# Kernel optimization log

Hardware: AMD Instinct MI355X
Metric: run time of the kernel (lower is better)

The kernel has to match this reference:

```python
import jax, jax.numpy as jnp
import numpy as np

T, B, C, H = 2048, 2, 1024, 16
DK = C // H


def setup_inputs() -> dict:
    key = jax.random.key(0)
    ks = jax.random.split(key, 12)
    s = 1.0 / np.sqrt(C)
    return {
        "query": jax.random.normal(ks[0], (T, B, C), jnp.float32),
        "key": jax.random.normal(ks[1], (T, B, C), jnp.float32),
        "value": jax.random.normal(ks[2], (T, B, C), jnp.float32),
        "Wq": jax.random.normal(ks[3], (C, C), jnp.float32) * s,
        "bq": jnp.zeros((C,), jnp.float32),
        "Wk": jax.random.normal(ks[4], (C, C), jnp.float32) * s,
        "bk": jnp.zeros((C,), jnp.float32),
        "Wv": jax.random.normal(ks[5], (C, C), jnp.float32) * s,
        "bv": jnp.zeros((C,), jnp.float32),
        "Wo": jax.random.normal(ks[6], (C, C), jnp.float32) * s,
        "bo": jnp.zeros((C,), jnp.float32),
        "key_padding_mask": jax.random.randint(ks[7], (B, T), 0, 2).astype(jnp.bool_),
    }


def reference(query, key, value, Wq, bq, Wk, bk, Wv, bv, Wo, bo, key_padding_mask):
    # T,B,C -> B,T,C
    q_in = jnp.transpose(query, (1, 0, 2))
    k_in = jnp.transpose(key, (1, 0, 2))
    v_in = jnp.transpose(value, (1, 0, 2))
    nb = q_in.shape[0]
    # linear projections, split heads: B,T,C -> B,H,T,dk
    def proj(x, W, b):
        y = x @ W.T + b
        return jnp.transpose(y.reshape(nb, -1, H, DK), (0, 2, 1, 3))
    q = proj(q_in, Wq, bq)
    k = proj(k_in, Wk, bk)
    v = proj(v_in, Wv, bv)
    # scores: B,H,T1,T2
    scores = jnp.einsum("bhqd,bhkd->bhqk", q, k) / np.sqrt(DK).astype(np.float32)
    scores = jnp.where(key_padding_mask[:, None, None, :], -jnp.inf, scores)
    attn = jax.nn.softmax(scores, axis=-1)
    # context: B,H,T1,dk -> B,T1,C
    x = jnp.einsum("bhqk,bhkd->bhqd", attn, v)
    x = jnp.transpose(x, (0, 2, 1, 3)).reshape(nb, -1, H * DK)
    out = x @ Wo.T + bo
    # B,T,C -> T,B,C
    return jnp.transpose(out, (1, 0, 2))
```

## Files before the change

kernel.cpp:

```cpp
#include <hip/hip_runtime.h>
#include <stdint.h>

typedef __attribute__((ext_vector_type(4))) float f32x4;
typedef __attribute__((ext_vector_type(16))) float f32x16;
typedef __attribute__((ext_vector_type(8))) short bf16x8;
typedef __attribute__((ext_vector_type(2))) unsigned int u32x2;
typedef __attribute__((ext_vector_type(4))) unsigned int u32x4;
typedef unsigned short u16;
typedef unsigned int u32;

#define DEVINL __device__ __forceinline__

DEVINL u16 f2bf(float f) {
  u32 u = __builtin_bit_cast(u32, f);
  u += 0x7FFFu + ((u >> 16) & 1u);
  return (u16)(u >> 16);
}

DEVINL float exp2_hw(float x) {
  float r;
  asm("v_exp_f32 %0, %1\n\ts_nop 0" : "=v"(r) : "v"(x));
  return r;
}

DEVINL u32 cvt_pk_bf16(float lo, float hi) {
  u32 r;
  asm("v_cvt_pk_bf16_f32 %0, %1, %2" : "=v"(r) : "v"(lo), "v"(hi));
  return r;
}

DEVINL void gload16(const void* g, void* l) {
  __builtin_amdgcn_global_load_lds((const __attribute__((address_space(1))) void*)g,
                                   (__attribute__((address_space(3))) void*)l, 16, 0, 0);
}

DEVINL void wait_vm0() { asm volatile("s_waitcnt vmcnt(0)" ::: "memory"); }
DEVINL void wait_vm3() { asm volatile("s_waitcnt vmcnt(3)" ::: "memory"); }
DEVINL void wait_vm4() { asm volatile("s_waitcnt vmcnt(4)" ::: "memory"); }
#define SBAR0 __builtin_amdgcn_sched_barrier(0)

__global__ void cvt_all(const float* __restrict__ q, const float* __restrict__ k,
                        const float* __restrict__ v, const float* __restrict__ wq,
                        const float* __restrict__ wk, const float* __restrict__ wv,
                        const float* __restrict__ wo, ushort4* __restrict__ dst,
                        const u32* __restrict__ mraw, float* __restrict__ mout) {
  if (blockIdx.x == 16384) {
    __shared__ int notint, notfloat;
    int tid = threadIdx.x;
    if (tid == 0) { notint = 0; notfloat = 0; }
    __syncthreads();
    for (int i = tid; i < 1024; i += 256) {
      u32 w = mraw[i];
      if (w != 0u && w != 1u) notint = 1;
      if (w != 0u && w != 0x3f800000u) notfloat = 1;
    }
    __syncthreads();
    bool words = (!notint) || (!notfloat);
    for (int i = tid; i < 4096; i += 256) {
      u32 vv = words ? mraw[i] : (u32)(((const unsigned char*)mraw)[i]);
      mout[i] = vv ? -1.0e38f : -8.0f;
    }
    return;
  }
  int i = blockIdx.x * 256 + threadIdx.x;
  float4 v4;
  if (i < 1048576) v4 = ((const float4*)q)[i];
  else if (i < 2097152) v4 = ((const float4*)k)[i - 1048576];
  else if (i < 3145728) v4 = ((const float4*)v)[i - 2097152];
  else {
    int j = i - 3145728;
    if (j < 262144) v4 = ((const float4*)wq)[j];
    else if (j < 524288) v4 = ((const float4*)wk)[j - 262144];
    else if (j < 786432) v4 = ((const float4*)wv)[j - 524288];
    else v4 = ((const float4*)wo)[j - 786432];
  }
  ushort4 o;
  o.x = f2bf(v4.x); o.y = f2bf(v4.y); o.z = f2bf(v4.z); o.w = f2bf(v4.w);
  dst[i] = o;
}

DEVINL void gemm_body(const u16* __restrict__ A, const u16* __restrict__ W,
                      const float* __restrict__ bias, u16* __restrict__ out_bf,
                      int tile, int mode, float scale, u16* As, u16* Bs) {
  const int tid = threadIdx.x, lane = tid & 63;
  const int wave = tid >> 6, wm = wave & 1, wn = wave >> 1;
  const int m0 = (tile >> 3) << 7;
  const int n0 = (tile & 7) << 7;
  const int l15 = lane & 15, l4 = lane >> 4;
  const int K = 1024;
  const f32x4 zero = {0.f, 0.f, 0.f, 0.f};
  f32x4 acc[4][4];
#pragma unroll
  for (int i = 0; i < 4; i++)
#pragma unroll
    for (int j = 0; j < 4; j++) acc[i][j] = zero;

  auto stage = [&](int buf, int kti) {
    u16* Ab = As + buf * 4096;
    u16* Bb = Bs + buf * 4096;
#pragma unroll
    for (int it = 0; it < 2; ++it) {
      int c = tid + (it << 8);
      int row = c >> 2, qs = (c & 3) ^ ((row & 3) ^ ((row >> 2) & 3));
      gload16(A + (size_t)(m0 + row) * K + kti * 32 + qs * 8, (void*)(Ab + c * 8));
      gload16(W + (size_t)(n0 + row) * K + kti * 32 + qs * 8, (void*)(Bb + c * 8));
    }
  };

  stage(0, 0);
  stage(1, 1);

  for (int kti = 0; kti < 32; ++kti) {
    const int cur = kti % 3;
    if (kti == 31) wait_vm0(); else wait_vm4();
    __builtin_amdgcn_s_barrier();
    SBAR0;
    if (kti < 30) stage((kti + 2) % 3, kti + 2);

    const u16* Ac = As + cur * 4096;
    const u16* Bc = Bs + cur * 4096;
    bf16x8 af[4], bfr[4];
#pragma unroll
    for (int i = 0; i < 4; i++) {
      int ra = (wm << 6) + (i << 4) + l15;
      int rb = (wn << 6) + (i << 4) + l15;
      af[i]  = *(const bf16x8*)(Ac + ra * 32 + ((l4 * 8) ^ ((((ra & 3) ^ ((ra >> 2) & 3))) << 3)));
      bfr[i] = *(const bf16x8*)(Bc + rb * 32 + ((l4 * 8) ^ ((((rb & 3) ^ ((rb >> 2) & 3))) << 3)));
    }
    __builtin_amdgcn_s_setprio(1);
#pragma unroll
    for (int i = 0; i < 4; i++)
#pragma unroll
      for (int j = 0; j < 4; j++)
        acc[i][j] = __builtin_amdgcn_mfma_f32_16x16x32_bf16(af[i], bfr[j], acc[i][j], 0, 0, 0);
    __builtin_amdgcn_s_setprio(0);
  }

#pragma unroll
  for (int j = 0; j < 4; j++) {
    const int col = n0 + (wn << 6) + (j << 4) + l15;
    const float bc = bias[col];
#pragma unroll
    for (int i = 0; i < 4; i++) {
#pragma unroll
      for (int r = 0; r < 4; r++) {
        const int row = m0 + (wm << 6) + (i << 4) + (l4 << 2) + r;
        float v = (acc[i][j][r] + bc) * scale;
        int t = row >> 1, b2 = row & 1, h = col >> 6, dh = col & 63;
        if (mode == 2)
          out_bf[((size_t)(b2 * 16 + h) * 64 + dh) * 2048 + t] = f2bf(v);
        else
          out_bf[((size_t)(b2 * 16 + h) * 2048 + t) * 64 + dh] = f2bf(v);
      }
    }
  }
}

__global__ __launch_bounds__(256, 3) void gemm_qkv(
    const u16* __restrict__ qbf, const u16* __restrict__ kbf, const u16* __restrict__ vbf,
    const u16* __restrict__ wq, const u16* __restrict__ wk, const u16* __restrict__ wv,
    const float* __restrict__ bq, const float* __restrict__ bk, const float* __restrict__ bv,
    u16* __restrict__ Qh, u16* __restrict__ Kh, u16* __restrict__ Vth) {
  __shared__ __align__(16) u16 As[3 * 4096];
  __shared__ __align__(16) u16 Bs[3 * 4096];
  const float C2 = 0.18033688011112042f;
  int wg = blockIdx.x;
  int swz = (wg & 7) * 96 + (wg >> 3);
  int prob = swz >> 8, tile = swz & 255;
  if (prob == 0)      gemm_body(qbf, wq, bq, Qh,  tile, 0, C2, As, Bs);
  else if (prob == 1) gemm_body(kbf, wk, bk, Kh,  tile, 0, 1.0f, As, Bs);
  else                gemm_body(vbf, wv, bv, Vth, tile, 2, 1.0f, As, Bs);
}

__global__ __launch_bounds__(256, 2) void gemm_o(
    const u16* __restrict__ ctx, const u16* __restrict__ wo,
    const float* __restrict__ bo, float* __restrict__ out) {
  __shared__ __align__(16) u16 As[3 * 2048];
  __shared__ __align__(16) u16 Bs[3 * 4096];
  const int tid = threadIdx.x, lane = tid & 63;
  const int wave = tid >> 6, wm = wave & 1, wn = wave >> 1;
  const int wg = blockIdx.x;
  const int swz = (wg & 7) * 64 + (wg >> 3);
  const int m0 = (swz >> 3) << 6;
  const int n0 = (swz & 7) << 7;
  const int l15 = lane & 15, l4 = lane >> 4;
  const f32x4 zero = {0.f, 0.f, 0.f, 0.f};
  f32x4 acc[2][4];
#pragma unroll
  for (int i = 0; i < 2; i++)
#pragma unroll
    for (int j = 0; j < 4; j++) acc[i][j] = zero;

  auto stage = [&](int buf, int kti) {
    u16* Ab = As + buf * 2048;
    u16* Bb = Bs + buf * 4096;
    {
      int c = tid;
      int row = c >> 2, qs = (c & 3) ^ ((row & 3) ^ ((row >> 2) & 3));
      gload16(ctx + (size_t)(m0 + row) * 1024 + kti * 32 + qs * 8, (void*)(Ab + c * 8));
    }
#pragma unroll
    for (int it = 0; it < 2; ++it) {
      int c = tid + (it << 8);
      int row = c >> 2, qs = (c & 3) ^ ((row & 3) ^ ((row >> 2) & 3));
      gload16(wo + (size_t)(n0 + row) * 1024 + kti * 32 + qs * 8, (void*)(Bb + c * 8));
    }
  };

  stage(0, 0);
  stage(1, 1);

  for (int kti = 0; kti < 32; ++kti) {
    const int cur = kti % 3;
    if (kti == 31) wait_vm0(); else wait_vm3();
    __builtin_amdgcn_s_barrier();
    SBAR0;
    if (kti < 30) stage((kti + 2) % 3, kti + 2);

    const u16* Ac = As + cur * 2048;
    const u16* Bc = Bs + cur * 4096;
    bf16x8 af[2], bfr[4];
#pragma unroll
    for (int i = 0; i < 2; i++) {
      int ra = (wm << 5) + (i << 4) + l15;
      af[i] = *(const bf16x8*)(Ac + ra * 32 + ((l4 * 8) ^ ((((ra & 3) ^ ((ra >> 2) & 3))) << 3)));
    }
#pragma unroll
    for (int j = 0; j < 4; j++) {
      int rb = (wn << 6) + (j << 4) + l15;
      bfr[j] = *(const bf16x8*)(Bc + rb * 32 + ((l4 * 8) ^ ((((rb & 3) ^ ((rb >> 2) & 3))) << 3)));
    }
    __builtin_amdgcn_s_setprio(1);
#pragma unroll
    for (int i = 0; i < 2; i++)
#pragma unroll
      for (int j = 0; j < 4; j++)
        acc[i][j] = __builtin_amdgcn_mfma_f32_16x16x32_bf16(af[i], bfr[j], acc[i][j], 0, 0, 0);
    __builtin_amdgcn_s_setprio(0);
  }

#pragma unroll
  for (int j = 0; j < 4; j++) {
    const int col = n0 + (wn << 6) + (j << 4) + l15;
    const float bc = bo[col];
#pragma unroll
    for (int i = 0; i < 2; i++) {
#pragma unroll
      for (int r = 0; r < 4; r++) {
        const int row = m0 + (wm << 5) + (i << 4) + (l4 << 2) + r;
        float v = acc[i][j][r] + bc;
        int t = row & 2047, b2 = row >> 11;
        out[(size_t)(t * 2 + b2) * 1024 + col] = v;
      }
    }
  }
}

__global__ __launch_bounds__(256, 2) void attn_fwd(
    const u16* __restrict__ Qh, const u16* __restrict__ Kh, const u16* __restrict__ Vt,
    const float* __restrict__ maskf, u16* __restrict__ ctx) {
  __shared__ __align__(16) u16 Ks[3][64 * 64];
  __shared__ __align__(16) u16 Vs[3][64 * 64];
  __shared__ __align__(16) float Ml[2048];
  const int tid = threadIdx.x, lane = tid & 63, wave = tid >> 6;
  const int wg = blockIdx.x;
  const int swz = (wg & 7) * 64 + (wg >> 3);
  const int qt = swz & 15, bh = swz >> 4;
  const int bb = bh >> 4, h = bh & 15;
  const int l31 = lane & 31, hi = lane >> 5;
  const size_t kvbase = (size_t)bh * 2048 * 64;
  const int qbase = qt * 128 + wave * 32;

  gload16(maskf + bb * 2048 + tid * 4, (void*)(&Ml[tid * 4]));
  gload16(maskf + bb * 2048 + 1024 + tid * 4, (void*)(&Ml[1024 + tid * 4]));

  bf16x8 qf[4];
#pragma unroll
  for (int kc = 0; kc < 4; kc++)
    qf[kc] = *(const bf16x8*)(Qh + kvbase + (size_t)(qbase + l31) * 64 + kc * 16 + hi * 8);

  f32x16 zz;
#pragma unroll
  for (int e = 0; e < 16; e++) zz[e] = 0.f;
  f32x16 O[2];
  O[0] = zz; O[1] = zz;
  float l_ = 0.f;

  auto stage = [&](int buf, int kt) {
#pragma unroll
    for (int it = 0; it < 2; ++it) {
      int c = tid + (it << 8);
      int row = c >> 3, qs = (c & 7) ^ (row & 7);
      gload16(Kh + kvbase + (size_t)(kt * 64 + row) * 64 + qs * 8, (void*)(&Ks[buf][c * 8]));
      gload16(Vt + kvbase + (size_t)row * 2048 + kt * 64 + qs * 8, (void*)(&Vs[buf][c * 8]));
    }
  };

  stage(0, 0);
  stage(1, 1);

  for (int kt = 0; kt < 32; ++kt) {
    const int cur = kt % 3;
    if (kt == 31) wait_vm0(); else wait_vm4();
    __builtin_amdgcn_s_barrier();
    SBAR0;
    if (kt < 30) stage((kt + 2) % 3, kt + 2);

    f32x16 s[2];
    s[0] = zz; s[1] = zz;
    __builtin_amdgcn_s_setprio(1);
#pragma unroll
    for (int kc = 0; kc < 4; kc++) {
      const int ch = (((kc * 2 + hi) ^ (l31 & 7)) << 3);
      bf16x8 kf0 = *(const bf16x8*)(&Ks[cur][l31 * 64 + ch]);
      bf16x8 kf1 = *(const bf16x8*)(&Ks[cur][(l31 + 32) * 64 + ch]);
      s[0] = __builtin_amdgcn_mfma_f32_32x32x16_bf16(kf0, qf[kc], s[0], 0, 0, 0);
      s[1] = __builtin_amdgcn_mfma_f32_32x32x16_bf16(kf1, qf[kc], s[1], 0, 0, 0);
    }
    __builtin_amdgcn_s_setprio(0);

    float rs = 0.f;
#pragma unroll
    for (int kb = 0; kb < 2; kb++)
#pragma unroll
      for (int g = 0; g < 4; g++) {
        float4 mv = *(const float4*)(&Ml[kt * 64 + kb * 32 + g * 8 + hi * 4]);
        float p0 = exp2_hw(s[kb][4 * g + 0] + mv.x);
        float p1 = exp2_hw(s[kb][4 * g + 1] + mv.y);
        float p2 = exp2_hw(s[kb][4 * g + 2] + mv.z);
        float p3 = exp2_hw(s[kb][4 * g + 3] + mv.w);
        s[kb][4 * g + 0] = p0; s[kb][4 * g + 1] = p1;
        s[kb][4 * g + 2] = p2; s[kb][4 * g + 3] = p3;
        rs += (p0 + p1) + (p2 + p3);
      }
    rs += __shfl_xor(rs, 32);
    l_ += rs;

    u32 pw[2][8];
#pragma unroll
    for (int kb = 0; kb < 2; kb++)
#pragma unroll
      for (int g = 0; g < 4; g++) {
        pw[kb][2 * g]     = cvt_pk_bf16(s[kb][4 * g + 0], s[kb][4 * g + 1]);
        pw[kb][2 * g + 1] = cvt_pk_bf16(s[kb][4 * g + 2], s[kb][4 * g + 3]);
      }

    __builtin_amdgcn_s_setprio(1);
#pragma unroll
    for (int kc = 0; kc < 4; kc++) {
      const int kb = kc >> 1, m = kc & 1;
      auto r0 = __builtin_amdgcn_permlane32_swap(pw[kb][4 * m + 0], pw[kb][4 * m + 2], false, false);
      auto r1 = __builtin_amdgcn_permlane32_swap(pw[kb][4 * m + 1], pw[kb][4 * m + 3], false, false);
      u32x4 fw = {r0[0], r1[0], r0[1], r1[1]};
      bf16x8 pf = __builtin_bit_cast(bf16x8, fw);
      const int ch = (((kc * 2 + hi) ^ (l31 & 7)) << 3);
      bf16x8 vf0 = *(const bf16x8*)(&Vs[cur][l31 * 64 + ch]);
      bf16x8 vf1 = *(const bf16x8*)(&Vs[cur][(l31 + 32) * 64 + ch]);
      O[0] = __builtin_amdgcn_mfma_f32_32x32x16_bf16(vf0, pf, O[0], 0, 0, 0);
      O[1] = __builtin_amdgcn_mfma_f32_32x32x16_bf16(vf1, pf, O[1], 0, 0, 0);
    }
    __builtin_amdgcn_s_setprio(0);
  }

  float inv = (l_ > 0.f) ? 1.0f / l_ : 0.f;
  const int q = qbase + l31;
  u16* cb = ctx + ((size_t)bb * 2048 + q) * 1024 + h * 64;
#pragma unroll
  for (int nd = 0; nd < 2; nd++)
#pragma unroll
    for (int g = 0; g < 4; g++) {
      u32x2 w;
      w[0] = cvt_pk_bf16(O[nd][4 * g + 0] * inv, O[nd][4 * g + 1] * inv);
      w[1] = cvt_pk_bf16(O[nd][4 * g + 2] * inv, O[nd][4 * g + 3] * inv);
      *(u32x2*)(cb + nd * 32 + g * 8 + hi * 4) = w;
    }
}

extern "C" void kernel_launch(void* const* d_in, const int* in_sizes, int n_in,
                              void* d_out, int out_size, void* d_ws, size_t ws_size,
                              hipStream_t stream) {
  const float* q_in = (const float*)d_in[0];
  const float* k_in = (const float*)d_in[1];
  const float* v_in = (const float*)d_in[2];
  const float* Wq = (const float*)d_in[3];
  const float* bq = (const float*)d_in[4];
  const float* Wk = (const float*)d_in[5];
  const float* bk = (const float*)d_in[6];
  const float* Wv = (const float*)d_in[7];
  const float* bv = (const float*)d_in[8];
  const float* Wo = (const float*)d_in[9];
  const float* bo = (const float*)d_in[10];
  const void* mask = d_in[11];

  const size_t SZ_X = (size_t)4194304 * 2;
  const size_t SZ_W = (size_t)1048576 * 2;
  uint8_t* ws = (uint8_t*)d_ws;
  float* mf = (float*)ws;
  size_t off = 32768;
  u16* qbf = (u16*)(ws + off); off += SZ_X;
  u16* kbf = (u16*)(ws + off); off += SZ_X;
  u16* vbf = (u16*)(ws + off); off += SZ_X;
  u16* wqb = (u16*)(ws + off); off += SZ_W;
  u16* wkb = (u16*)(ws + off); off += SZ_W;
  u16* wvb = (u16*)(ws + off); off += SZ_W;
  u16* wob = (u16*)(ws + off); off += SZ_W;
  u16* Qh  = (u16*)(ws + off); off += SZ_X;
  u16* Kh  = (u16*)(ws + off); off += SZ_X;
  u16* Vth = (u16*)(ws + off); off += SZ_X;
  u16* ctx = (u16*)(ws + off); off += SZ_X;
  if (ws_size < off) return;

  cvt_all<<<16385, 256, 0, stream>>>(q_in, k_in, v_in, Wq, Wk, Wv, Wo,
                                     (ushort4*)qbf, (const u32*)mask, mf);

  gemm_qkv<<<768, 256, 0, stream>>>(qbf, kbf, vbf, wqb, wkb, wvb, bq, bk, bv, Qh, Kh, Vth);

  attn_fwd<<<512, 256, 0, stream>>>(Qh, Kh, Vth, mf, ctx);

  gemm_o<<<512, 256, 0, stream>>>(ctx, wob, bo, (float*)d_out);
}
```

Measured before the change: 134.8 us.

## Rewrite attention kernel with 16x16 MFMA tiles, smaller query blocks, double buffering

The attention kernel moves from 32x32x16 MFMA on 128-query blocks to 16x16x32 MFMA on 64-query blocks, which doubles the grid and raises the launch-bounds occupancy target. The K/V staging ring drops from a triple buffer with vmcnt waits to a double buffer with a full __syncthreads per tile. The probability transpose goes through a per-wave swizzled LDS scratch instead of permlane32 swaps, and the mask is read straight from global memory rather than staged in LDS. The aim is more waves in flight to hide latency. In exchange, each K/V tile is reused across fewer queries, and the kernel adds barriers and LDS round trips.

```diff
diff --git a/kernel.cpp b/kernel.cpp
--- a/kernel.cpp
+++ b/kernel.cpp
@@ -2,7 +2,6 @@
 #include <stdint.h>
 
 typedef __attribute__((ext_vector_type(4))) float f32x4;
-typedef __attribute__((ext_vector_type(16))) float f32x16;
 typedef __attribute__((ext_vector_type(8))) short bf16x8;
 typedef __attribute__((ext_vector_type(2))) unsigned int u32x2;
 typedef __attribute__((ext_vector_type(4))) unsigned int u32x4;
@@ -256,34 +255,29 @@
   }
 }
 
-__global__ __launch_bounds__(256, 2) void attn_fwd(
+__global__ __launch_bounds__(256, 4) void attn_fwd(
     const u16* __restrict__ Qh, const u16* __restrict__ Kh, const u16* __restrict__ Vt,
     const float* __restrict__ maskf, u16* __restrict__ ctx) {
-  __shared__ __align__(16) u16 Ks[3][64 * 64];
-  __shared__ __align__(16) u16 Vs[3][64 * 64];
-  __shared__ __align__(16) float Ml[2048];
+  __shared__ __align__(16) u16 Ks[2][64 * 64];
+  __shared__ __align__(16) u16 Vs[2][64 * 64];
+  __shared__ __align__(16) u32 Plu[4][16 * 32];
   const int tid = threadIdx.x, lane = tid & 63, wave = tid >> 6;
   const int wg = blockIdx.x;
-  const int swz = (wg & 7) * 64 + (wg >> 3);
-  const int qt = swz & 15, bh = swz >> 4;
+  const int swz = (wg & 7) * 128 + (wg >> 3);
+  const int qt = swz & 31, bh = swz >> 5;
   const int bb = bh >> 4, h = bh & 15;
-  const int l31 = lane & 31, hi = lane >> 5;
+  const int l15 = lane & 15, l4 = lane >> 4;
+  const f32x4 zero = {0.f, 0.f, 0.f, 0.f};
   const size_t kvbase = (size_t)bh * 2048 * 64;
-  const int qbase = qt * 128 + wave * 32;
-
-  gload16(maskf + bb * 2048 + tid * 4, (void*)(&Ml[tid * 4]));
-  gload16(maskf + bb * 2048 + 1024 + tid * 4, (void*)(&Ml[1024 + tid * 4]));
-
-  bf16x8 qf[4];
-#pragma unroll
-  for (int kc = 0; kc < 4; kc++)
-    qf[kc] = *(const bf16x8*)(Qh + kvbase + (size_t)(qbase + l31) * 64 + kc * 16 + hi * 8);
-
-  f32x16 zz;
-#pragma unroll
-  for (int e = 0; e < 16; e++) zz[e] = 0.f;
-  f32x16 O[2];
-  O[0] = zz; O[1] = zz;
+
+  bf16x8 qf[2];
+#pragma unroll
+  for (int kb = 0; kb < 2; kb++)
+    qf[kb] = *(const bf16x8*)(Qh + kvbase + (size_t)(qt * 64 + wave * 16 + l15) * 64 + kb * 32 + l4 * 8);
+
+  f32x4 O[4];
+#pragma unroll
+  for (int nd = 0; nd < 4; nd++) O[nd] = zero;
   float l_ = 0.f;
 
   auto stage = [&](int buf, int kt) {
@@ -297,83 +291,83 @@
   };
 
   stage(0, 0);
-  stage(1, 1);
+  __syncthreads();
+
+  const float4* mrow = (const float4*)(maskf + bb * 2048);
 
   for (int kt = 0; kt < 32; ++kt) {
-    const int cur = kt % 3;
-    if (kt == 31) wait_vm0(); else wait_vm4();
-    __builtin_amdgcn_s_barrier();
-    SBAR0;
-    if (kt < 30) stage((kt + 2) % 3, kt + 2);
-
-    f32x16 s[2];
-    s[0] = zz; s[1] = zz;
+    const int cur = kt & 1;
+    if (kt < 31) stage(cur ^ 1, kt + 1);
+
+    f32x4 s[4];
     __builtin_amdgcn_s_setprio(1);
 #pragma unroll
-    for (int kc = 0; kc < 4; kc++) {
-      const int ch = (((kc * 2 + hi) ^ (l31 & 7)) << 3);
-      bf16x8 kf0 = *(const bf16x8*)(&Ks[cur][l31 * 64 + ch]);
-      bf16x8 kf1 = *(const bf16x8*)(&Ks[cur][(l31 + 32) * 64 + ch]);
-      s[0] = __builtin_amdgcn_mfma_f32_32x32x16_bf16(kf0, qf[kc], s[0], 0, 0, 0);
-      s[1] = __builtin_amdgcn_mfma_f32_32x32x16_bf16(kf1, qf[kc], s[1], 0, 0, 0);
+    for (int ni = 0; ni < 4; ni++) {
+      int row = ni * 16 + l15;
+      s[ni] = zero;
+#pragma unroll
+      for (int kb = 0; kb < 2; kb++) {
+        bf16x8 kf = *(const bf16x8*)(&Ks[cur][row * 64 + (((kb * 64 + l4 * 16) ^ ((row & 7) << 4)) >> 1)]);
+        s[ni] = __builtin_amdgcn_mfma_f32_16x16x32_bf16(kf, qf[kb], s[ni], 0, 0, 0);
+      }
     }
     __builtin_amdgcn_s_setprio(0);
 
     float rs = 0.f;
 #pragma unroll
-    for (int kb = 0; kb < 2; kb++)
-#pragma unroll
-      for (int g = 0; g < 4; g++) {
-        float4 mv = *(const float4*)(&Ml[kt * 64 + kb * 32 + g * 8 + hi * 4]);
-        float p0 = exp2_hw(s[kb][4 * g + 0] + mv.x);
-        float p1 = exp2_hw(s[kb][4 * g + 1] + mv.y);
-        float p2 = exp2_hw(s[kb][4 * g + 2] + mv.z);
-        float p3 = exp2_hw(s[kb][4 * g + 3] + mv.w);
-        s[kb][4 * g + 0] = p0; s[kb][4 * g + 1] = p1;
-        s[kb][4 * g + 2] = p2; s[kb][4 * g + 3] = p3;
-        rs += (p0 + p1) + (p2 + p3);
-      }
+    for (int ni = 0; ni < 4; ni++) {
+      float4 mv = mrow[kt * 16 + ni * 4 + l4];
+      float p0 = exp2_hw(s[ni][0] + mv.x);
+      float p1 = exp2_hw(s[ni][1] + mv.y);
+      float p2 = exp2_hw(s[ni][2] + mv.z);
+      float p3 = exp2_hw(s[ni][3] + mv.w);
+      s[ni][0] = p0; s[ni][1] = p1; s[ni][2] = p2; s[ni][3] = p3;
+      rs += (p0 + p1) + (p2 + p3);
+    }
+    rs += __shfl_xor(rs, 16);
     rs += __shfl_xor(rs, 32);
     l_ += rs;
 
-    u32 pw[2][8];
-#pragma unroll
-    for (int kb = 0; kb < 2; kb++)
-#pragma unroll
-      for (int g = 0; g < 4; g++) {
-        pw[kb][2 * g]     = cvt_pk_bf16(s[kb][4 * g + 0], s[kb][4 * g + 1]);
-        pw[kb][2 * g + 1] = cvt_pk_bf16(s[kb][4 * g + 2], s[kb][4 * g + 3]);
+#pragma unroll
+    for (int ni = 0; ni < 4; ni++) {
+      u32x2 w;
+      w.x = cvt_pk_bf16(s[ni][0], s[ni][1]);
+      w.y = cvt_pk_bf16(s[ni][2], s[ni][3]);
+      int col = ni * 8 + l4 * 2;
+      *(u32x2*)(&Plu[wave][l15 * 32 + (col ^ ((l15 & 7) << 2))]) = w;
+    }
+
+    bf16x8 pb[2];
+#pragma unroll
+    for (int kb = 0; kb < 2; kb++) {
+      int rcol = kb * 16 + l4 * 4;
+      pb[kb] = *(const bf16x8*)(&Plu[wave][l15 * 32 + (rcol ^ ((l15 & 7) << 2))]);
+    }
+    __builtin_amdgcn_s_setprio(1);
+#pragma unroll
+    for (int nd = 0; nd < 4; nd++) {
+      int row = nd * 16 + l15;
+#pragma unroll
+      for (int jb = 0; jb < 2; jb++) {
+        bf16x8 vf = *(const bf16x8*)(&Vs[cur][row * 64 + (((jb * 64 + l4 * 16) ^ ((row & 7) << 4)) >> 1)]);
+        O[nd] = __builtin_amdgcn_mfma_f32_16x16x32_bf16(vf, pb[jb], O[nd], 0, 0, 0);
       }
-
-    __builtin_amdgcn_s_setprio(1);
-#pragma unroll
-    for (int kc = 0; kc < 4; kc++) {
-      const int kb = kc >> 1, m = kc & 1;
-      auto r0 = __builtin_amdgcn_permlane32_swap(pw[kb][4 * m + 0], pw[kb][4 * m + 2], false, false);
-      auto r1 = __builtin_amdgcn_permlane32_swap(pw[kb][4 * m + 1], pw[kb][4 * m + 3], false, false);
-      u32x4 fw = {r0[0], r1[0], r0[1], r1[1]};
-      bf16x8 pf = __builtin_bit_cast(bf16x8, fw);
-      const int ch = (((kc * 2 + hi) ^ (l31 & 7)) << 3);
-      bf16x8 vf0 = *(const bf16x8*)(&Vs[cur][l31 * 64 + ch]);
-      bf16x8 vf1 = *(const bf16x8*)(&Vs[cur][(l31 + 32) * 64 + ch]);
-      O[0] = __builtin_amdgcn_mfma_f32_32x32x16_bf16(vf0, pf, O[0], 0, 0, 0);
-      O[1] = __builtin_amdgcn_mfma_f32_32x32x16_bf16(vf1, pf, O[1], 0, 0, 0);
     }
     __builtin_amdgcn_s_setprio(0);
+
+    __syncthreads();
   }
 
   float inv = (l_ > 0.f) ? 1.0f / l_ : 0.f;
-  const int q = qbase + l31;
-  u16* cb = ctx + ((size_t)bb * 2048 + q) * 1024 + h * 64;
-#pragma unroll
-  for (int nd = 0; nd < 2; nd++)
-#pragma unroll
-    for (int g = 0; g < 4; g++) {
-      u32x2 w;
-      w[0] = cvt_pk_bf16(O[nd][4 * g + 0] * inv, O[nd][4 * g + 1] * inv);
-      w[1] = cvt_pk_bf16(O[nd][4 * g + 2] * inv, O[nd][4 * g + 3] * inv);
-      *(u32x2*)(cb + nd * 32 + g * 8 + hi * 4) = w;
-    }
+  int t = qt * 64 + wave * 16 + l15;
+  u16* cb = ctx + ((size_t)bb * 2048 + t) * 1024 + h * 64;
+#pragma unroll
+  for (int nd = 0; nd < 4; nd++) {
+    u32x2 w;
+    w.x = cvt_pk_bf16(O[nd][0] * inv, O[nd][1] * inv);
+    w.y = cvt_pk_bf16(O[nd][2] * inv, O[nd][3] * inv);
+    *(u32x2*)(cb + nd * 16 + l4 * 4) = w;
+  }
 }
 
 extern "C" void kernel_launch(void* const* d_in, const int* in_sizes, int n_in,
@@ -415,7 +409,7 @@
 
   gemm_qkv<<<768, 256, 0, stream>>>(qbf, kbf, vbf, wqb, wkb, wvb, bq, bk, bv, Qh, Kh, Vth);
 
-  attn_fwd<<<512, 256, 0, stream>>>(Qh, Kh, Vth, mf, ctx);
+  attn_fwd<<<1024, 256, 0, stream>>>(Qh, Kh, Vth, mf, ctx);
 
   gemm_o<<<512, 256, 0, stream>>>(ctx, wob, bo, (float*)d_out);
 }
```

Result: slower. 142.8 us (+6.0%).

## Software-pipeline QK^T of next key tile with softmax and PV of current

Applied to the files above, without the earlier changes.

The attention loop is restructured so each iteration issues the QK^T MFMAs for the next key tile before running the exp/softmax and PV MFMAs for the current tile, with two ping-pong score registers. The K/V LDS ring goes from 3 to 4 buffers and prefetch runs three tiles ahead, with wait counts adjusted. The goal is to overlap matrix-core work with the transcendental and conversion ALU work and hide load latency better. In exchange it uses more LDS per block and more accumulator registers, which could cost occupancy or cause spills.

```diff
diff --git a/kernel.cpp b/kernel.cpp
--- a/kernel.cpp
+++ b/kernel.cpp
@@ -37,6 +37,7 @@
 DEVINL void wait_vm0() { asm volatile("s_waitcnt vmcnt(0)" ::: "memory"); }
 DEVINL void wait_vm3() { asm volatile("s_waitcnt vmcnt(3)" ::: "memory"); }
 DEVINL void wait_vm4() { asm volatile("s_waitcnt vmcnt(4)" ::: "memory"); }
+DEVINL void wait_vm8() { asm volatile("s_waitcnt vmcnt(8)" ::: "memory"); }
 #define SBAR0 __builtin_amdgcn_sched_barrier(0)
 
 __global__ void cvt_all(const float* __restrict__ q, const float* __restrict__ k,
@@ -259,8 +260,8 @@
 __global__ __launch_bounds__(256, 2) void attn_fwd(
     const u16* __restrict__ Qh, const u16* __restrict__ Kh, const u16* __restrict__ Vt,
     const float* __restrict__ maskf, u16* __restrict__ ctx) {
-  __shared__ __align__(16) u16 Ks[3][64 * 64];
-  __shared__ __align__(16) u16 Vs[3][64 * 64];
+  __shared__ __align__(16) u16 Ks[4][64 * 64];
+  __shared__ __align__(16) u16 Vs[4][64 * 64];
   __shared__ __align__(16) float Ml[2048];
   const int tid = threadIdx.x, lane = tid & 63, wave = tid >> 6;
   const int wg = blockIdx.x;
@@ -274,18 +275,6 @@
   gload16(maskf + bb * 2048 + tid * 4, (void*)(&Ml[tid * 4]));
   gload16(maskf + bb * 2048 + 1024 + tid * 4, (void*)(&Ml[1024 + tid * 4]));
 
-  bf16x8 qf[4];
-#pragma unroll
-  for (int kc = 0; kc < 4; kc++)
-    qf[kc] = *(const bf16x8*)(Qh + kvbase + (size_t)(qbase + l31) * 64 + kc * 16 + hi * 8);
-
-  f32x16 zz;
-#pragma unroll
-  for (int e = 0; e < 16; e++) zz[e] = 0.f;
-  f32x16 O[2];
-  O[0] = zz; O[1] = zz;
-  float l_ = 0.f;
-
   auto stage = [&](int buf, int kt) {
 #pragma unroll
     for (int it = 0; it < 2; ++it) {
@@ -298,53 +287,71 @@
 
   stage(0, 0);
   stage(1, 1);
-
-  for (int kt = 0; kt < 32; ++kt) {
-    const int cur = kt % 3;
-    if (kt == 31) wait_vm0(); else wait_vm4();
+  stage(2, 2);
+
+  bf16x8 qf[4];
+#pragma unroll
+  for (int kc = 0; kc < 4; kc++)
+    qf[kc] = *(const bf16x8*)(Qh + kvbase + (size_t)(qbase + l31) * 64 + kc * 16 + hi * 8);
+
+  f32x16 zz;
+#pragma unroll
+  for (int e = 0; e < 16; e++) zz[e] = 0.f;
+  f32x16 O[2];
+  O[0] = zz; O[1] = zz;
+  float l_ = 0.f;
+
+  auto qk = [&](int buf, f32x16& s0, f32x16& s1) {
+    s0 = zz; s1 = zz;
+#pragma unroll
+    for (int kc = 0; kc < 4; kc++) {
+      const int ch = (((kc * 2 + hi) ^ (l31 & 7)) << 3);
+      bf16x8 kf0 = *(const bf16x8*)(&Ks[buf][l31 * 64 + ch]);
+      bf16x8 kf1 = *(const bf16x8*)(&Ks[buf][(l31 + 32) * 64 + ch]);
+      s0 = __builtin_amdgcn_mfma_f32_32x32x16_bf16(kf0, qf[kc], s0, 0, 0, 0);
+      s1 = __builtin_amdgcn_mfma_f32_32x32x16_bf16(kf1, qf[kc], s1, 0, 0, 0);
+    }
+  };
+
+  auto iter = [&](int kt, f32x16& c0, f32x16& c1, f32x16& n0, f32x16& n1) {
+    if (kt == 30) wait_vm0(); else wait_vm4();
     __builtin_amdgcn_s_barrier();
     SBAR0;
-    if (kt < 30) stage((kt + 2) % 3, kt + 2);
-
-    f32x16 s[2];
-    s[0] = zz; s[1] = zz;
-    __builtin_amdgcn_s_setprio(1);
-#pragma unroll
-    for (int kc = 0; kc < 4; kc++) {
-      const int ch = (((kc * 2 + hi) ^ (l31 & 7)) << 3);
-      bf16x8 kf0 = *(const bf16x8*)(&Ks[cur][l31 * 64 + ch]);
-      bf16x8 kf1 = *(const bf16x8*)(&Ks[cur][(l31 + 32) * 64 + ch]);
-      s[0] = __builtin_amdgcn_mfma_f32_32x32x16_bf16(kf0, qf[kc], s[0], 0, 0, 0);
-      s[1] = __builtin_amdgcn_mfma_f32_32x32x16_bf16(kf1, qf[kc], s[1], 0, 0, 0);
-    }
-    __builtin_amdgcn_s_setprio(0);
+    if (kt <= 28) stage((kt + 3) & 3, kt + 3);
+    if (kt < 31) qk((kt + 1) & 3, n0, n1);
 
     float rs = 0.f;
-#pragma unroll
-    for (int kb = 0; kb < 2; kb++)
+    f32x16* sp[2] = {&c0, &c1};
+#pragma unroll
+    for (int kb = 0; kb < 2; kb++) {
+      f32x16& s = *sp[kb];
 #pragma unroll
       for (int g = 0; g < 4; g++) {
         float4 mv = *(const float4*)(&Ml[kt * 64 + kb * 32 + g * 8 + hi * 4]);
-        float p0 = exp2_hw(s[kb][4 * g + 0] + mv.x);
-        float p1 = exp2_hw(s[kb][4 * g + 1] + mv.y);
-        float p2 = exp2_hw(s[kb][4 * g + 2] + mv.z);
-        float p3 = exp2_hw(s[kb][4 * g + 3] + mv.w);
-        s[kb][4 * g + 0] = p0; s[kb][4 * g + 1] = p1;
-        s[kb][4 * g + 2] = p2; s[kb][4 * g + 3] = p3;
+        float p0 = exp2_hw(s[4 * g + 0] + mv.x);
+        float p1 = exp2_hw(s[4 * g + 1] + mv.y);
+        float p2 = exp2_hw(s[4 * g + 2] + mv.z);
+        float p3 = exp2_hw(s[4 * g + 3] + mv.w);
+        s[4 * g + 0] = p0; s[4 * g + 1] = p1;
+        s[4 * g + 2] = p2; s[4 * g + 3] = p3;
         rs += (p0 + p1) + (p2 + p3);
       }
+    }
     rs += __shfl_xor(rs, 32);
     l_ += rs;
 
     u32 pw[2][8];
 #pragma unroll
-    for (int kb = 0; kb < 2; kb++)
+    for (int kb = 0; kb < 2; kb++) {
+      f32x16& s = *sp[kb];
 #pragma unroll
       for (int g = 0; g < 4; g++) {
-        pw[kb][2 * g]     = cvt_pk_bf16(s[kb][4 * g + 0], s[kb][4 * g + 1]);
-        pw[kb][2 * g + 1] = cvt_pk_bf16(s[kb][4 * g + 2], s[kb][4 * g + 3]);
+        pw[kb][2 * g]     = cvt_pk_bf16(s[4 * g + 0], s[4 * g + 1]);
+        pw[kb][2 * g + 1] = cvt_pk_bf16(s[4 * g + 2], s[4 * g + 3]);
       }
-
+    }
+
+    const int cur = kt & 3;
     __builtin_amdgcn_s_setprio(1);
 #pragma unroll
     for (int kc = 0; kc < 4; kc++) {
@@ -360,6 +367,17 @@
       O[1] = __builtin_amdgcn_mfma_f32_32x32x16_bf16(vf1, pf, O[1], 0, 0, 0);
     }
     __builtin_amdgcn_s_setprio(0);
+  };
+
+  wait_vm8();
+  __builtin_amdgcn_s_barrier();
+  SBAR0;
+  f32x16 sA0, sA1, sB0, sB1;
+  qk(0, sA0, sA1);
+
+  for (int kp = 0; kp < 16; ++kp) {
+    iter(2 * kp,     sA0, sA1, sB0, sB1);
+    iter(2 * kp + 1, sB0, sB1, sA0, sA1);
   }
 
   float inv = (l_ > 0.f) ? 1.0f / l_ : 0.f;
```

Result: no change. 134.1 us (-0.5%).
